# Optimization experiments

Measured on AMD Instinct MI355X. Metric: run time of the kernel, lower is better.

## Reference

```python
import jax, jax.numpy as jnp
import numpy as np

G, M_PER_GROUP, K, N = 8, 2048, 4096, 4096  # experts, tokens/expert, d_model, expert out dim


def setup_inputs() -> dict:
    key = jax.random.key(0)
    k1, k2, k3, k4 = jax.random.split(key, 4)
    T = G * M_PER_GROUP
    # int8 quantized activations [total_tokens, K] and per-expert weights [G, N, K] ('NT' layout)
    i8_left_tensor = jax.random.randint(k1, (T, K), -127, 128, dtype=jnp.int32).astype(jnp.int8)
    i8_right_tensors = jax.random.randint(k2, (G, N, K), -127, 128, dtype=jnp.int32).astype(jnp.int8)
    # per-token and per-(group, out-channel) dequant scales
    left_scales = jax.random.uniform(k3, (T,), jnp.float32, 0.001, 0.02)
    right_scales = jax.random.uniform(k4, (G, N), jnp.float32, 0.001, 0.02)
    tokens_per_group = jnp.full((G,), M_PER_GROUP, dtype=jnp.int32)
    return {
        "i8_left_tensor": i8_left_tensor,
        "i8_right_tensors": i8_right_tensors,
        "left_scales": left_scales,
        "right_scales": right_scales,
        "tokens_per_group": tokens_per_group,
    }


def reference(i8_left_tensor, i8_right_tensors, left_scales, right_scales, tokens_per_group):
    # moe_w8a8_group_gemm, 'NT': per group g, out_g = (A_g @ B_g^T) * ls_g[:, None] * rs_g[None, :] -> fp16
    g, n, k = i8_right_tensors.shape
    t = i8_left_tensor.shape[0]
    m = t // g  # equal-sized groups (tokens_per_group is constant M_PER_GROUP)
    a = i8_left_tensor.reshape(g, m, k).astype(jnp.float32)   # [G, M, K]
    b = i8_right_tensors.astype(jnp.float32)                  # [G, N, K]
    acc = jnp.einsum('gmk,gnk->gmn', a, b)                    # int8xint8 accum in f32
    ls = left_scales.reshape(g, m, 1)
    rs = right_scales[:, None, :]
    out = (acc * ls * rs).astype(jnp.float16)                 # fused dequant epilogue
    return out.reshape(t, n)
```

## Files before the change

### kernel.cpp

```cpp
#include <hip/hip_runtime.h>

#define GG 8
#define MPG 2048
#define KD 4096
#define ND 4096

using i32x4 = __attribute__((ext_vector_type(4))) int;

__device__ __forceinline__ int pack4(i32x4 v) {
  return (int)((unsigned)(v[0] & 0xff) | ((unsigned)(v[1] & 0xff) << 8) |
               ((unsigned)(v[2] & 0xff) << 16) | ((unsigned)(v[3] & 0xff) << 24));
}

__global__ void conv_kernel(const int* __restrict__ src, char* __restrict__ dst, long nelem) {
  long t = (long)blockIdx.x * blockDim.x + threadIdx.x;
  long stride = (long)gridDim.x * blockDim.x;
  for (long e = t * 16; e < nelem; e += stride * 16) {
    i32x4 x0 = *(const i32x4*)(src + e);
    i32x4 x1 = *(const i32x4*)(src + e + 4);
    i32x4 x2 = *(const i32x4*)(src + e + 8);
    i32x4 x3 = *(const i32x4*)(src + e + 12);
    i32x4 p;
    p[0] = pack4(x0); p[1] = pack4(x1); p[2] = pack4(x2); p[3] = pack4(x3);
    *(i32x4*)(dst + e) = p;
  }
}

__device__ __forceinline__ void gload_lds16(const void* g, void* l) {
  __builtin_amdgcn_global_load_lds(
      (const __attribute__((address_space(1))) unsigned int*)g,
      (__attribute__((address_space(3))) unsigned int*)l, 16, 0, 0);
}

#define CFENCE() asm volatile("" ::: "memory")

constexpr int NT = KD / 128;

__global__ __launch_bounds__(512, 2) void gemm256_i8(
    const char* __restrict__ Aall,
    const char* __restrict__ Ball,
    const float* __restrict__ ls,
    const float* __restrict__ rs,
    float* __restrict__ out,
    int g0, int nwg)
{
  extern __shared__ char lds[];

  const int tid  = threadIdx.x;
  const int lane = tid & 63;
  const int wave = tid >> 6;

  int bid = blockIdx.x;
  int wg  = (bid & 7) * (nwg >> 3) + (bid >> 3);
  const int gl = wg >> 7;
  const int rr_ = wg & 127;
  const int bm = (rr_ >> 4) * 256;
  const int bn = (rr_ & 15) * 256;
  const int g  = g0 + gl;

  const int srow = tid >> 3;
  const int scol = ((tid & 7) << 4) ^ ((srow & 7) << 4);
  const char* Ag = Aall + ((size_t)gl * MPG + bm) * KD;
  const char* Bg = Ball + ((size_t)gl * ND  + bn) * KD;
  const char* pa[4]; const char* pb[4];
#pragma unroll
  for (int i = 0; i < 4; ++i) {
    pa[i] = Ag + (size_t)(i * 64 + srow) * KD + scol;
    pb[i] = Bg + (size_t)(i * 64 + srow) * KD + scol;
  }
  char* wbase = lds + wave * 1024;

  auto stageA = [&](int buf, int kt) {
    const int ko = kt << 7;
    char* d = wbase + buf * 65536;
#pragma unroll
    for (int i = 0; i < 4; ++i) gload_lds16(pa[i] + ko, d + i * 8192);
  };
  auto stageB = [&](int buf, int kt) {
    const int ko = kt << 7;
    char* d = wbase + buf * 65536 + 32768;
#pragma unroll
    for (int i = 0; i < 4; ++i) gload_lds16(pb[i] + ko, d + i * 8192);
  };

  const int wm = wave >> 2;
  const int wn = wave & 3;
  const int r16 = lane & 15;
  const int klane = (lane >> 4) << 4;
  const int sx = (r16 & 7) << 4;
  const char* aBase0 = lds + (size_t)(wm * 128 + r16) * 128;
  const char* bBase0 = lds + 32768 + (size_t)(wn * 64 + r16) * 128;

  i32x4 acc[8][4] = {};

  stageA(0, 0); stageB(0, 0);
  asm volatile("s_waitcnt vmcnt(0)" ::: "memory");
  __builtin_amdgcn_s_barrier();
  CFENCE();

#pragma unroll 1
  for (int kt = 0; kt < NT; ++kt) {
    const int c = kt & 1;
    const char* pA = aBase0 + c * 65536;
    const char* pB = bBase0 + c * 65536;
    const int kx0 = klane ^ sx;
    const int kx1 = (64 + klane) ^ sx;
    const bool pre = (kt + 1 < NT);
    i32x4 af[4], bf[4];

#pragma unroll
    for (int n = 0; n < 4; ++n) bf[n] = *(const i32x4*)(pB + n * 2048 + kx0);
#pragma unroll
    for (int m = 0; m < 4; ++m) af[m] = *(const i32x4*)(pA + m * 2048 + kx0);
    if (pre) stageA(c ^ 1, kt + 1);
    CFENCE(); __builtin_amdgcn_s_barrier(); CFENCE();
    __builtin_amdgcn_s_setprio(1);
#pragma unroll
    for (int m = 0; m < 4; ++m)
#pragma unroll
      for (int n = 0; n < 4; ++n)
        acc[m][n] = __builtin_amdgcn_mfma_i32_16x16x64_i8(af[m], bf[n], acc[m][n], 0, 0, 0);
    __builtin_amdgcn_s_setprio(0);
    CFENCE(); __builtin_amdgcn_s_barrier(); CFENCE();

#pragma unroll
    for (int m = 0; m < 4; ++m) af[m] = *(const i32x4*)(pA + (4 + m) * 2048 + kx0);
    if (pre) stageB(c ^ 1, kt + 1);
    CFENCE(); __builtin_amdgcn_s_barrier(); CFENCE();
    __builtin_amdgcn_s_setprio(1);
#pragma unroll
    for (int m = 0; m < 4; ++m)
#pragma unroll
      for (int n = 0; n < 4; ++n)
        acc[4 + m][n] = __builtin_amdgcn_mfma_i32_16x16x64_i8(af[m], bf[n], acc[4 + m][n], 0, 0, 0);
    __builtin_amdgcn_s_setprio(0);
    CFENCE(); __builtin_amdgcn_s_barrier(); CFENCE();

#pragma unroll
    for (int n = 0; n < 4; ++n) bf[n] = *(const i32x4*)(pB + n * 2048 + kx1);
#pragma unroll
    for (int m = 0; m < 4; ++m) af[m] = *(const i32x4*)(pA + m * 2048 + kx1);
    CFENCE(); __builtin_amdgcn_s_barrier(); CFENCE();
    __builtin_amdgcn_s_setprio(1);
#pragma unroll
    for (int m = 0; m < 4; ++m)
#pragma unroll
      for (int n = 0; n < 4; ++n)
        acc[m][n] = __builtin_amdgcn_mfma_i32_16x16x64_i8(af[m], bf[n], acc[m][n], 0, 0, 0);
    __builtin_amdgcn_s_setprio(0);
    CFENCE(); __builtin_amdgcn_s_barrier(); CFENCE();

#pragma unroll
    for (int m = 0; m < 4; ++m) af[m] = *(const i32x4*)(pA + (4 + m) * 2048 + kx1);
    asm volatile("s_waitcnt vmcnt(0)" ::: "memory");
    CFENCE(); __builtin_amdgcn_s_barrier(); CFENCE();
    __builtin_amdgcn_s_setprio(1);
#pragma unroll
    for (int m = 0; m < 4; ++m)
#pragma unroll
      for (int n = 0; n < 4; ++n)
        acc[4 + m][n] = __builtin_amdgcn_mfma_i32_16x16x64_i8(af[m], bf[n], acc[4 + m][n], 0, 0, 0);
    __builtin_amdgcn_s_setprio(0);
    CFENCE(); __builtin_amdgcn_s_barrier(); CFENCE();
  }

  const size_t orow0 = (size_t)g * MPG + bm + wm * 128 + ((lane >> 4) << 2);
  const int col0 = bn + wn * 64 + r16;
  float rsv[4];
#pragma unroll
  for (int n = 0; n < 4; ++n) rsv[n] = rs[(size_t)g * ND + col0 + n * 16];
#pragma unroll
  for (int m = 0; m < 8; ++m) {
#pragma unroll
    for (int q = 0; q < 4; ++q) {
      size_t row = orow0 + m * 16 + q;
      float lsv = ls[row];
#pragma unroll
      for (int n = 0; n < 4; ++n)
        out[row * ND + col0 + n * 16] = (float)acc[m][n][q] * lsv * rsv[n];
    }
  }
}

constexpr int BM = 128, BN = 128, BK = 64;

template<bool DIRECT>
__global__ __launch_bounds__(256) void gemm_i8(
    const void* __restrict__ Aptr, const void* __restrict__ Bptr,
    const float* __restrict__ ls, const float* __restrict__ rs,
    float* __restrict__ out, int g0)
{
  __shared__ char lA[BM * BK];
  __shared__ char lB[BN * BK];

  const int gl = blockIdx.z;
  const int g = g0 + gl;
  const int bm = blockIdx.y * BM;
  const int bn = blockIdx.x * BN;
  const int tid = threadIdx.x;
  const int lane = tid & 63;
  const int wave = tid >> 6;
  const int wr = (wave >> 1) * 64;
  const int wc = (wave & 1) * 64;
  const int r16 = lane & 15;
  const int kb = (lane >> 4) * 16;

  i32x4 acc[4][4] = {};

  if constexpr (!DIRECT) {
    const char* Ag = (const char*)Aptr + ((size_t)gl * MPG + bm) * KD;
    const char* Bg = (const char*)Bptr + ((size_t)gl * ND + bn) * KD;
    const int srow = tid >> 2;
    const int skoff = (tid & 3) * 16;
    const char* pa0 = Ag + (size_t)srow * KD + skoff;
    const char* pa1 = Ag + (size_t)(srow + 64) * KD + skoff;
    const char* pb0 = Bg + (size_t)srow * KD + skoff;
    const char* pb1 = Bg + (size_t)(srow + 64) * KD + skoff;
    char* la0 = lA + wave * 1024;
    char* la1 = lA + 4096 + wave * 1024;
    char* lb0 = lB + wave * 1024;
    char* lb1 = lB + 4096 + wave * 1024;

    for (int k0 = 0; k0 < KD; k0 += BK) {
      gload_lds16(pa0 + k0, la0);
      gload_lds16(pa1 + k0, la1);
      gload_lds16(pb0 + k0, lb0);
      gload_lds16(pb1 + k0, lb1);
      __syncthreads();
      i32x4 af[4], bf[4];
#pragma unroll
      for (int m = 0; m < 4; ++m) af[m] = *(const i32x4*)(lA + (wr + m * 16 + r16) * BK + kb);
#pragma unroll
      for (int n = 0; n < 4; ++n) bf[n] = *(const i32x4*)(lB + (wc + n * 16 + r16) * BK + kb);
#pragma unroll
      for (int m = 0; m < 4; ++m)
#pragma unroll
        for (int n = 0; n < 4; ++n)
          acc[m][n] = __builtin_amdgcn_mfma_i32_16x16x64_i8(af[m], bf[n], acc[m][n], 0, 0, 0);
      __syncthreads();
    }
  } else {
    const int* Ag = (const int*)Aptr + ((size_t)gl * MPG + bm) * KD;
    const int* Bg = (const int*)Bptr + ((size_t)gl * ND + bn) * KD;
    const int drow = tid >> 1;
    const int dk = (tid & 1) * 32;

    for (int k0 = 0; k0 < KD; k0 += BK) {
      int pa[8], pb[8];
#pragma unroll
      for (int j = 0; j < 8; ++j) pa[j] = pack4(*(const i32x4*)(Ag + (size_t)drow * KD + k0 + dk + j * 4));
#pragma unroll
      for (int j = 0; j < 8; ++j) pb[j] = pack4(*(const i32x4*)(Bg + (size_t)drow * KD + k0 + dk + j * 4));
      __syncthreads();
      *(i32x4*)(lA + drow * 64 + dk)      = *(i32x4*)(pa);
      *(i32x4*)(lA + drow * 64 + dk + 16) = *(i32x4*)(pa + 4);
      *(i32x4*)(lB + drow * 64 + dk)      = *(i32x4*)(pb);
      *(i32x4*)(lB + drow * 64 + dk + 16) = *(i32x4*)(pb + 4);
      __syncthreads();
      i32x4 af[4], bf[4];
#pragma unroll
      for (int m = 0; m < 4; ++m) af[m] = *(const i32x4*)(lA + (wr + m * 16 + r16) * BK + kb);
#pragma unroll
      for (int n = 0; n < 4; ++n) bf[n] = *(const i32x4*)(lB + (wc + n * 16 + r16) * BK + kb);
#pragma unroll
      for (int m = 0; m < 4; ++m)
#pragma unroll
        for (int n = 0; n < 4; ++n)
          acc[m][n] = __builtin_amdgcn_mfma_i32_16x16x64_i8(af[m], bf[n], acc[m][n], 0, 0, 0);
    }
  }

  const size_t trow0 = (size_t)g * MPG + bm + wr + (lane >> 4) * 4;
  const int col0 = bn + wc + r16;
  float rsv[4];
#pragma unroll
  for (int n = 0; n < 4; ++n) rsv[n] = rs[(size_t)g * ND + col0 + n * 16];
#pragma unroll
  for (int m = 0; m < 4; ++m) {
#pragma unroll
    for (int q = 0; q < 4; ++q) {
      size_t row = trow0 + m * 16 + q;
      float lsv = ls[row];
#pragma unroll
      for (int n = 0; n < 4; ++n)
        out[row * ND + col0 + n * 16] = (float)acc[m][n][q] * lsv * rsv[n];
    }
  }
}

extern "C" void kernel_launch(void* const* d_in, const int* in_sizes, int n_in,
                              void* d_out, int out_size, void* d_ws, size_t ws_size,
                              hipStream_t stream) {
  const int* A32 = (const int*)d_in[0];
  const int* B32 = (const int*)d_in[1];
  const float* ls = (const float*)d_in[2];
  const float* rs = (const float*)d_in[3];
  float* out = (float*)d_out;

  const size_t aE = (size_t)GG * MPG * KD;
  const size_t bE = (size_t)GG * ND * KD;
  const size_t aSlab = (size_t)MPG * KD;
  const size_t bSlab = (size_t)ND * KD;

  const int smem = 131072;
  bool big_lds_ok =
      hipFuncSetAttribute((const void*)gemm256_i8,
                          hipFuncAttributeMaxDynamicSharedMemorySize, smem) == hipSuccess;

  if (d_ws && ws_size >= aE + bE) {
    char* wsA = (char*)d_ws;
    char* wsB = wsA + aE;
    conv_kernel<<<8192, 256, 0, stream>>>(A32, wsA, (long)aE);
    conv_kernel<<<16384, 256, 0, stream>>>(B32, wsB, (long)bE);
    if (big_lds_ok) {
      gemm256_i8<<<1024, 512, smem, stream>>>(wsA, wsB, ls, rs, out, 0, 1024);
    } else {
      dim3 grid(ND / BN, MPG / BM, GG);
      gemm_i8<false><<<grid, dim3(256), 0, stream>>>(wsA, wsB, ls, rs, out, 0);
    }
  } else if (d_ws && ws_size >= aSlab + bSlab) {
    char* wsA = (char*)d_ws;
    char* wsB = wsA + aSlab;
    for (int gidx = 0; gidx < GG; ++gidx) {
      conv_kernel<<<2048, 256, 0, stream>>>(A32 + (size_t)gidx * aSlab, wsA, (long)aSlab);
      conv_kernel<<<4096, 256, 0, stream>>>(B32 + (size_t)gidx * bSlab, wsB, (long)bSlab);
      if (big_lds_ok) {
        gemm256_i8<<<128, 512, smem, stream>>>(wsA, wsB, ls, rs, out, gidx, 128);
      } else {
        dim3 grid(ND / BN, MPG / BM, 1);
        gemm_i8<false><<<grid, dim3(256), 0, stream>>>(wsA, wsB, ls, rs, out, gidx);
      }
    }
  } else {
    dim3 grid(ND / BN, MPG / BM, GG);
    gemm_i8<true><<<grid, dim3(256), 0, stream>>>(A32, B32, ls, rs, out, 0);
  }
}
```

Measured before the change: 484.5 us.

## Deepen global-to-LDS prefetch to two tiles ahead and cut barriers per k-step

Restructures the main loop so global-to-LDS loads for tile kt+2 are issued at the end of iteration kt, instead of staging the next tile halfway through the current one. Each iteration now waits on vmcnt(8) and a single barrier up front, then runs all four MFMA sub-blocks with extra fragment registers (double A/B fragments) in place of eight interleaved barriers. The aim is to hide global latency better and remove barrier stalls, at the cost of more VGPRs. It relies on the vmcnt count matching exactly the number of outstanding loads for one tile, and on the buffer being reused only after every wave has finished reading it.

```diff
diff --git a/kernel.cpp b/kernel.cpp
--- a/kernel.cpp
+++ b/kernel.cpp
@@ -94,9 +94,7 @@
   i32x4 acc[8][4] = {};
 
   stageA(0, 0); stageB(0, 0);
-  asm volatile("s_waitcnt vmcnt(0)" ::: "memory");
-  __builtin_amdgcn_s_barrier();
-  CFENCE();
+  stageA(1, 1); stageB(1, 1);
 
 #pragma unroll 1
   for (int kt = 0; kt < NT; ++kt) {
@@ -105,63 +103,57 @@
     const char* pB = bBase0 + c * 65536;
     const int kx0 = klane ^ sx;
     const int kx1 = (64 + klane) ^ sx;
-    const bool pre = (kt + 1 < NT);
-    i32x4 af[4], bf[4];
-
-#pragma unroll
-    for (int n = 0; n < 4; ++n) bf[n] = *(const i32x4*)(pB + n * 2048 + kx0);
-#pragma unroll
-    for (int m = 0; m < 4; ++m) af[m] = *(const i32x4*)(pA + m * 2048 + kx0);
-    if (pre) stageA(c ^ 1, kt + 1);
-    CFENCE(); __builtin_amdgcn_s_barrier(); CFENCE();
+
+    if (kt + 1 < NT) { asm volatile("s_waitcnt vmcnt(8)" ::: "memory"); }
+    else             { asm volatile("s_waitcnt vmcnt(0)" ::: "memory"); }
+    __builtin_amdgcn_s_barrier();
+    CFENCE();
+
+    i32x4 bf0[4], bf1[4], af0[4], af1[4];
+#pragma unroll
+    for (int n = 0; n < 4; ++n) bf0[n] = *(const i32x4*)(pB + n * 2048 + kx0);
+#pragma unroll
+    for (int m = 0; m < 4; ++m) af0[m] = *(const i32x4*)(pA + m * 2048 + kx0);
+#pragma unroll
+    for (int m = 0; m < 4; ++m) af1[m] = *(const i32x4*)(pA + (4 + m) * 2048 + kx0);
     __builtin_amdgcn_s_setprio(1);
 #pragma unroll
     for (int m = 0; m < 4; ++m)
 #pragma unroll
       for (int n = 0; n < 4; ++n)
-        acc[m][n] = __builtin_amdgcn_mfma_i32_16x16x64_i8(af[m], bf[n], acc[m][n], 0, 0, 0);
+        acc[m][n] = __builtin_amdgcn_mfma_i32_16x16x64_i8(af0[m], bf0[n], acc[m][n], 0, 0, 0);
     __builtin_amdgcn_s_setprio(0);
-    CFENCE(); __builtin_amdgcn_s_barrier(); CFENCE();
-
-#pragma unroll
-    for (int m = 0; m < 4; ++m) af[m] = *(const i32x4*)(pA + (4 + m) * 2048 + kx0);
-    if (pre) stageB(c ^ 1, kt + 1);
-    CFENCE(); __builtin_amdgcn_s_barrier(); CFENCE();
+#pragma unroll
+    for (int n = 0; n < 4; ++n) bf1[n] = *(const i32x4*)(pB + n * 2048 + kx1);
+#pragma unroll
+    for (int m = 0; m < 4; ++m) af0[m] = *(const i32x4*)(pA + m * 2048 + kx1);
     __builtin_amdgcn_s_setprio(1);
 #pragma unroll
     for (int m = 0; m < 4; ++m)
 #pragma unroll
       for (int n = 0; n < 4; ++n)
-        acc[4 + m][n] = __builtin_amdgcn_mfma_i32_16x16x64_i8(af[m], bf[n], acc[4 + m][n], 0, 0, 0);
+        acc[4 + m][n] = __builtin_amdgcn_mfma_i32_16x16x64_i8(af1[m], bf0[n], acc[4 + m][n], 0, 0, 0);
     __builtin_amdgcn_s_setprio(0);
-    CFENCE(); __builtin_amdgcn_s_barrier(); CFENCE();
-
-#pragma unroll
-    for (int n = 0; n < 4; ++n) bf[n] = *(const i32x4*)(pB + n * 2048 + kx1);
-#pragma unroll
-    for (int m = 0; m < 4; ++m) af[m] = *(const i32x4*)(pA + m * 2048 + kx1);
-    CFENCE(); __builtin_amdgcn_s_barrier(); CFENCE();
+#pragma unroll
+    for (int m = 0; m < 4; ++m) af1[m] = *(const i32x4*)(pA + (4 + m) * 2048 + kx1);
     __builtin_amdgcn_s_setprio(1);
 #pragma unroll
     for (int m = 0; m < 4; ++m)
 #pragma unroll
       for (int n = 0; n < 4; ++n)
-        acc[m][n] = __builtin_amdgcn_mfma_i32_16x16x64_i8(af[m], bf[n], acc[m][n], 0, 0, 0);
+        acc[m][n] = __builtin_amdgcn_mfma_i32_16x16x64_i8(af0[m], bf1[n], acc[m][n], 0, 0, 0);
+#pragma unroll
+    for (int m = 0; m < 4; ++m)
+#pragma unroll
+      for (int n = 0; n < 4; ++n)
+        acc[4 + m][n] = __builtin_amdgcn_mfma_i32_16x16x64_i8(af1[m], bf1[n], acc[4 + m][n], 0, 0, 0);
     __builtin_amdgcn_s_setprio(0);
-    CFENCE(); __builtin_amdgcn_s_barrier(); CFENCE();
-
-#pragma unroll
-    for (int m = 0; m < 4; ++m) af[m] = *(const i32x4*)(pA + (4 + m) * 2048 + kx1);
-    asm volatile("s_waitcnt vmcnt(0)" ::: "memory");
-    CFENCE(); __builtin_amdgcn_s_barrier(); CFENCE();
-    __builtin_amdgcn_s_setprio(1);
-#pragma unroll
-    for (int m = 0; m < 4; ++m)
-#pragma unroll
-      for (int n = 0; n < 4; ++n)
-        acc[4 + m][n] = __builtin_amdgcn_mfma_i32_16x16x64_i8(af[m], bf[n], acc[4 + m][n], 0, 0, 0);
-    __builtin_amdgcn_s_setprio(0);
-    CFENCE(); __builtin_amdgcn_s_barrier(); CFENCE();
+
+    asm volatile("s_waitcnt lgkmcnt(0)" ::: "memory");
+    __builtin_amdgcn_sched_barrier(0);
+    __builtin_amdgcn_s_barrier();
+    CFENCE();
+    if (kt + 2 < NT) { stageA(c, kt + 2); stageB(c, kt + 2); }
   }
 
   const size_t orow0 = (size_t)g * MPG + bm + wm * 128 + ((lane >> 4) << 2);
```

New measurement: 496.6 us. 2.5% more time.

## Fuse int8 conversion and grouped GEMM into one cooperative persistent kernel

Applied to the files above, without the earlier changes.

Replaces the separate conversion and GEMM launches with a single cooperative kernel. 128 blocks pack the int32 inputs to int8 group by group and publish per-group completion flags, while 384 persistent blocks run 256x128 tiles and spin-wait on those flags, so conversion of later groups overlaps GEMM on earlier ones. The new tile uses a single LDS buffer with 256 threads (48KB LDS), making stage loads synchronous with compute, and relies on atomic flag polling with a bounded spin. Fewer GEMM blocks and no double buffering could reduce GEMM throughput compared with the previous 512-thread double-buffered kernel.

```diff
diff --git a/kernel.cpp b/kernel.cpp
--- a/kernel.cpp
+++ b/kernel.cpp
@@ -12,18 +12,20 @@
                ((unsigned)(v[2] & 0xff) << 16) | ((unsigned)(v[3] & 0xff) << 24));
 }
 
+__device__ __forceinline__ void pack16(const int* __restrict__ src, char* __restrict__ dst, long e) {
+  i32x4 x0 = *(const i32x4*)(src + e);
+  i32x4 x1 = *(const i32x4*)(src + e + 4);
+  i32x4 x2 = *(const i32x4*)(src + e + 8);
+  i32x4 x3 = *(const i32x4*)(src + e + 12);
+  i32x4 p;
+  p[0] = pack4(x0); p[1] = pack4(x1); p[2] = pack4(x2); p[3] = pack4(x3);
+  *(i32x4*)(dst + e) = p;
+}
+
 __global__ void conv_kernel(const int* __restrict__ src, char* __restrict__ dst, long nelem) {
   long t = (long)blockIdx.x * blockDim.x + threadIdx.x;
-  long stride = (long)gridDim.x * blockDim.x;
-  for (long e = t * 16; e < nelem; e += stride * 16) {
-    i32x4 x0 = *(const i32x4*)(src + e);
-    i32x4 x1 = *(const i32x4*)(src + e + 4);
-    i32x4 x2 = *(const i32x4*)(src + e + 8);
-    i32x4 x3 = *(const i32x4*)(src + e + 12);
-    i32x4 p;
-    p[0] = pack4(x0); p[1] = pack4(x1); p[2] = pack4(x2); p[3] = pack4(x3);
-    *(i32x4*)(dst + e) = p;
-  }
+  long stride = (long)gridDim.x * blockDim.x * 16;
+  for (long e = t * 16; e < nelem; e += stride) pack16(src, dst, e);
 }
 
 __device__ __forceinline__ void gload_lds16(const void* g, void* l) {
@@ -34,34 +36,210 @@
 
 #define CFENCE() asm volatile("" ::: "memory")
 
-constexpr int NT = KD / 128;
-
-__global__ __launch_bounds__(512, 2) void gemm256_i8(
-    const char* __restrict__ Aall,
-    const char* __restrict__ Ball,
-    const float* __restrict__ ls,
-    const float* __restrict__ rs,
-    float* __restrict__ out,
-    int g0, int nwg)
+constexpr long A_EL = (long)MPG * KD;
+constexpr long B_EL = (long)ND * KD;
+constexpr int NTK = KD / 128;
+constexpr int NGEMM_B = 384;
+constexpr int NCONV_B = 128;
+constexpr int NTILES = GG * 256;
+
+__device__ __forceinline__ void gemm_tile(
+    char* lds, const char* __restrict__ Ag8, const char* __restrict__ Bg8,
+    const float* __restrict__ ls, const float* __restrict__ rs,
+    float* __restrict__ out, int g, int bm, int bn)
+{
+  const int tid = threadIdx.x;
+  const int lane = tid & 63;
+  const int wave = tid >> 6;
+
+  const int srow = tid >> 3;
+  const int scol = ((tid & 7) << 4) ^ ((srow & 7) << 4);
+  const char* Ag = Ag8 + (size_t)bm * KD;
+  const char* Bg = Bg8 + (size_t)bn * KD;
+  const int voff = srow * KD + scol;
+  char* wbase = lds + wave * 1024;
+
+  auto stage = [&](int kt) {
+    const int ko = kt << 7;
+#pragma unroll
+    for (int i = 0; i < 8; ++i)
+      gload_lds16(Ag + (size_t)(ko + voff) + (size_t)i * (32 * KD), wbase + i * 4096);
+#pragma unroll
+    for (int i = 0; i < 4; ++i)
+      gload_lds16(Bg + (size_t)(ko + voff) + (size_t)i * (32 * KD), wbase + 32768 + i * 4096);
+  };
+
+  const int wm = wave >> 1;
+  const int wn = wave & 1;
+  const int r16 = lane & 15;
+  const int klane = (lane >> 4) << 4;
+  const int sx = (r16 & 7) << 4;
+  const char* pA = lds + (size_t)(wm * 128 + r16) * 128;
+  const char* pB = lds + 32768 + (size_t)(wn * 64 + r16) * 128;
+  const int kx0 = klane ^ sx;
+  const int kx1 = (64 + klane) ^ sx;
+
+  i32x4 acc[8][4] = {};
+
+  stage(0);
+  asm volatile("s_waitcnt vmcnt(0)" ::: "memory");
+  __builtin_amdgcn_s_barrier();
+  CFENCE();
+
+#pragma unroll 1
+  for (int kt = 0; kt < NTK; ++kt) {
+    i32x4 bf0[4], bf1[4], af0[4], af1[4];
+#pragma unroll
+    for (int n = 0; n < 4; ++n) bf0[n] = *(const i32x4*)(pB + n * 2048 + kx0);
+#pragma unroll
+    for (int m = 0; m < 4; ++m) af0[m] = *(const i32x4*)(pA + m * 2048 + kx0);
+#pragma unroll
+    for (int m = 0; m < 4; ++m) af1[m] = *(const i32x4*)(pA + (4 + m) * 2048 + kx0);
+    __builtin_amdgcn_s_setprio(1);
+#pragma unroll
+    for (int m = 0; m < 4; ++m)
+#pragma unroll
+      for (int n = 0; n < 4; ++n)
+        acc[m][n] = __builtin_amdgcn_mfma_i32_16x16x64_i8(af0[m], bf0[n], acc[m][n], 0, 0, 0);
+    __builtin_amdgcn_s_setprio(0);
+#pragma unroll
+    for (int n = 0; n < 4; ++n) bf1[n] = *(const i32x4*)(pB + n * 2048 + kx1);
+#pragma unroll
+    for (int m = 0; m < 4; ++m) af0[m] = *(const i32x4*)(pA + m * 2048 + kx1);
+    __builtin_amdgcn_s_setprio(1);
+#pragma unroll
+    for (int m = 0; m < 4; ++m)
+#pragma unroll
+      for (int n = 0; n < 4; ++n)
+        acc[4 + m][n] = __builtin_amdgcn_mfma_i32_16x16x64_i8(af1[m], bf0[n], acc[4 + m][n], 0, 0, 0);
+    __builtin_amdgcn_s_setprio(0);
+#pragma unroll
+    for (int m = 0; m < 4; ++m) af1[m] = *(const i32x4*)(pA + (4 + m) * 2048 + kx1);
+    __builtin_amdgcn_s_setprio(1);
+#pragma unroll
+    for (int m = 0; m < 4; ++m)
+#pragma unroll
+      for (int n = 0; n < 4; ++n)
+        acc[m][n] = __builtin_amdgcn_mfma_i32_16x16x64_i8(af0[m], bf1[n], acc[m][n], 0, 0, 0);
+#pragma unroll
+    for (int m = 0; m < 4; ++m)
+#pragma unroll
+      for (int n = 0; n < 4; ++n)
+        acc[4 + m][n] = __builtin_amdgcn_mfma_i32_16x16x64_i8(af1[m], bf1[n], acc[4 + m][n], 0, 0, 0);
+    __builtin_amdgcn_s_setprio(0);
+
+    asm volatile("s_waitcnt lgkmcnt(0)" ::: "memory");
+    __builtin_amdgcn_sched_barrier(0);
+    __builtin_amdgcn_s_barrier();
+    CFENCE();
+    if (kt + 1 < NTK) stage(kt + 1);
+    asm volatile("s_waitcnt vmcnt(0)" ::: "memory");
+    __builtin_amdgcn_s_barrier();
+    CFENCE();
+  }
+
+  const size_t orow0 = (size_t)g * MPG + bm + wm * 128 + ((lane >> 4) << 2);
+  const int col0 = bn + wn * 64 + r16;
+  float rsv[4];
+#pragma unroll
+  for (int n = 0; n < 4; ++n) rsv[n] = rs[(size_t)g * ND + col0 + n * 16];
+#pragma unroll
+  for (int m = 0; m < 8; ++m) {
+#pragma unroll
+    for (int q = 0; q < 4; ++q) {
+      size_t row = orow0 + m * 16 + q;
+      float lsv = ls[row];
+#pragma unroll
+      for (int n = 0; n < 4; ++n)
+        out[row * ND + col0 + n * 16] = (float)acc[m][n][q] * lsv * rsv[n];
+    }
+  }
+}
+
+__global__ __launch_bounds__(256, 2) void mega_i8(
+    const int* __restrict__ A32, const int* __restrict__ B32,
+    char* __restrict__ wsA, char* __restrict__ wsB,
+    const float* __restrict__ ls, const float* __restrict__ rs,
+    float* __restrict__ out, int* __restrict__ flags)
 {
   extern __shared__ char lds[];
-
-  const int tid  = threadIdx.x;
+  const int tid = threadIdx.x;
+
+  if (blockIdx.x >= NGEMM_B) {
+    const int cb = blockIdx.x - NGEMM_B;
+    const long nthr = (long)NCONV_B * 256;
+    const long t0 = (long)cb * 256 + tid;
+    for (int g = 0; g < GG; ++g) {
+      {
+        const int* src = A32 + (size_t)g * A_EL;
+        char* dst = wsA + (size_t)g * A_EL;
+        for (long e = t0 * 64; e < A_EL; e += nthr * 64) {
+          pack16(src, dst, e);      pack16(src, dst, e + 16);
+          pack16(src, dst, e + 32); pack16(src, dst, e + 48);
+        }
+      }
+      {
+        const int* src = B32 + (size_t)g * B_EL;
+        char* dst = wsB + (size_t)g * B_EL;
+        for (long e = t0 * 64; e < B_EL; e += nthr * 64) {
+          pack16(src, dst, e);      pack16(src, dst, e + 16);
+          pack16(src, dst, e + 32); pack16(src, dst, e + 48);
+        }
+      }
+      __threadfence();
+      __syncthreads();
+      if (tid == 0) {
+        if (atomicAdd(&flags[1 + g], 1) == NCONV_B - 1)
+          atomicAdd(&flags[0], 1);
+      }
+    }
+    return;
+  }
+
+  const int b = blockIdx.x;
+  const int bs = (b & 7) * (NGEMM_B / 8) + (b >> 3);
+#pragma unroll 1
+  for (int t = bs; t < NTILES; t += NGEMM_B) {
+    const int grp = t >> 8;
+    const int idx = t & 255;
+    const int bm = (idx >> 5) * 256;
+    const int bn = (idx & 31) * 128;
+    if (tid == 0) {
+      int cap = 0;
+      while (atomicAdd(&flags[0], 0) < grp + 1) {
+        __builtin_amdgcn_s_sleep(2);
+        if (++cap > 5000000) break;
+      }
+    }
+    __syncthreads();
+    __threadfence();
+    gemm_tile(lds, wsA + (size_t)grp * A_EL, wsB + (size_t)grp * B_EL,
+              ls, rs, out, grp, bm, bn);
+  }
+}
+
+__global__ __launch_bounds__(512, 2) void gemm256sq_i8(
+    const char* __restrict__ Aall, const char* __restrict__ Ball,
+    const float* __restrict__ ls, const float* __restrict__ rs,
+    float* __restrict__ out, int g0, int nwg)
+{
+  extern __shared__ char lds[];
+  const int tid = threadIdx.x;
   const int lane = tid & 63;
   const int wave = tid >> 6;
 
   int bid = blockIdx.x;
-  int wg  = (bid & 7) * (nwg >> 3) + (bid >> 3);
+  int wg = (bid & 7) * (nwg >> 3) + (bid >> 3);
   const int gl = wg >> 7;
   const int rr_ = wg & 127;
   const int bm = (rr_ >> 4) * 256;
   const int bn = (rr_ & 15) * 256;
-  const int g  = g0 + gl;
+  const int g = g0 + gl;
 
   const int srow = tid >> 3;
   const int scol = ((tid & 7) << 4) ^ ((srow & 7) << 4);
   const char* Ag = Aall + ((size_t)gl * MPG + bm) * KD;
-  const char* Bg = Ball + ((size_t)gl * ND  + bn) * KD;
+  const char* Bg = Ball + ((size_t)gl * ND + bn) * KD;
   const char* pa[4]; const char* pb[4];
 #pragma unroll
   for (int i = 0; i < 4; ++i) {
@@ -99,13 +277,13 @@
   CFENCE();
 
 #pragma unroll 1
-  for (int kt = 0; kt < NT; ++kt) {
+  for (int kt = 0; kt < NTK; ++kt) {
     const int c = kt & 1;
     const char* pA = aBase0 + c * 65536;
     const char* pB = bBase0 + c * 65536;
     const int kx0 = klane ^ sx;
     const int kx1 = (64 + klane) ^ sx;
-    const bool pre = (kt + 1 < NT);
+    const bool pre = (kt + 1 < NTK);
     i32x4 af[4], bf[4];
 
 #pragma unroll
@@ -174,112 +352,6 @@
 #pragma unroll
     for (int q = 0; q < 4; ++q) {
       size_t row = orow0 + m * 16 + q;
-      float lsv = ls[row];
-#pragma unroll
-      for (int n = 0; n < 4; ++n)
-        out[row * ND + col0 + n * 16] = (float)acc[m][n][q] * lsv * rsv[n];
-    }
-  }
-}
-
-constexpr int BM = 128, BN = 128, BK = 64;
-
-template<bool DIRECT>
-__global__ __launch_bounds__(256) void gemm_i8(
-    const void* __restrict__ Aptr, const void* __restrict__ Bptr,
-    const float* __restrict__ ls, const float* __restrict__ rs,
-    float* __restrict__ out, int g0)
-{
-  __shared__ char lA[BM * BK];
-  __shared__ char lB[BN * BK];
-
-  const int gl = blockIdx.z;
-  const int g = g0 + gl;
-  const int bm = blockIdx.y * BM;
-  const int bn = blockIdx.x * BN;
-  const int tid = threadIdx.x;
-  const int lane = tid & 63;
-  const int wave = tid >> 6;
-  const int wr = (wave >> 1) * 64;
-  const int wc = (wave & 1) * 64;
-  const int r16 = lane & 15;
-  const int kb = (lane >> 4) * 16;
-
-  i32x4 acc[4][4] = {};
-
-  if constexpr (!DIRECT) {
-    const char* Ag = (const char*)Aptr + ((size_t)gl * MPG + bm) * KD;
-    const char* Bg = (const char*)Bptr + ((size_t)gl * ND + bn) * KD;
-    const int srow = tid >> 2;
-    const int skoff = (tid & 3) * 16;
-    const char* pa0 = Ag + (size_t)srow * KD + skoff;
-    const char* pa1 = Ag + (size_t)(srow + 64) * KD + skoff;
-    const char* pb0 = Bg + (size_t)srow * KD + skoff;
-    const char* pb1 = Bg + (size_t)(srow + 64) * KD + skoff;
-    char* la0 = lA + wave * 1024;
-    char* la1 = lA + 4096 + wave * 1024;
-    char* lb0 = lB + wave * 1024;
-    char* lb1 = lB + 4096 + wave * 1024;
-
-    for (int k0 = 0; k0 < KD; k0 += BK) {
-      gload_lds16(pa0 + k0, la0);
-      gload_lds16(pa1 + k0, la1);
-      gload_lds16(pb0 + k0, lb0);
-      gload_lds16(pb1 + k0, lb1);
-      __syncthreads();
-      i32x4 af[4], bf[4];
-#pragma unroll
-      for (int m = 0; m < 4; ++m) af[m] = *(const i32x4*)(lA + (wr + m * 16 + r16) * BK + kb);
-#pragma unroll
-      for (int n = 0; n < 4; ++n) bf[n] = *(const i32x4*)(lB + (wc + n * 16 + r16) * BK + kb);
-#pragma unroll
-      for (int m = 0; m < 4; ++m)
-#pragma unroll
-        for (int n = 0; n < 4; ++n)
-          acc[m][n] = __builtin_amdgcn_mfma_i32_16x16x64_i8(af[m], bf[n], acc[m][n], 0, 0, 0);
-      __syncthreads();
-    }
-  } else {
-    const int* Ag = (const int*)Aptr + ((size_t)gl * MPG + bm) * KD;
-    const int* Bg = (const int*)Bptr + ((size_t)gl * ND + bn) * KD;
-    const int drow = tid >> 1;
-    const int dk = (tid & 1) * 32;
-
-    for (int k0 = 0; k0 < KD; k0 += BK) {
-      int pa[8], pb[8];
-#pragma unroll
-      for (int j = 0; j < 8; ++j) pa[j] = pack4(*(const i32x4*)(Ag + (size_t)drow * KD + k0 + dk + j * 4));
-#pragma unroll
-      for (int j = 0; j < 8; ++j) pb[j] = pack4(*(const i32x4*)(Bg + (size_t)drow * KD + k0 + dk + j * 4));
-      __syncthreads();
-      *(i32x4*)(lA + drow * 64 + dk)      = *(i32x4*)(pa);
-      *(i32x4*)(lA + drow * 64 + dk + 16) = *(i32x4*)(pa + 4);
-      *(i32x4*)(lB + drow * 64 + dk)      = *(i32x4*)(pb);
-      *(i32x4*)(lB + drow * 64 + dk + 16) = *(i32x4*)(pb + 4);
-      __syncthreads();
-      i32x4 af[4], bf[4];
-#pragma unroll
-      for (int m = 0; m < 4; ++m) af[m] = *(const i32x4*)(lA + (wr + m * 16 + r16) * BK + kb);
-#pragma unroll
-      for (int n = 0; n < 4; ++n) bf[n] = *(const i32x4*)(lB + (wc + n * 16 + r16) * BK + kb);
-#pragma unroll
-      for (int m = 0; m < 4; ++m)
-#pragma unroll
-        for (int n = 0; n < 4; ++n)
-          acc[m][n] = __builtin_amdgcn_mfma_i32_16x16x64_i8(af[m], bf[n], acc[m][n], 0, 0, 0);
-    }
-  }
-
-  const size_t trow0 = (size_t)g * MPG + bm + wr + (lane >> 4) * 4;
-  const int col0 = bn + wc + r16;
-  float rsv[4];
-#pragma unroll
-  for (int n = 0; n < 4; ++n) rsv[n] = rs[(size_t)g * ND + col0 + n * 16];
-#pragma unroll
-  for (int m = 0; m < 4; ++m) {
-#pragma unroll
-    for (int q = 0; q < 4; ++q) {
-      size_t row = trow0 + m * 16 + q;
       float lsv = ls[row];
 #pragma unroll
       for (int n = 0; n < 4; ++n)
@@ -297,42 +369,63 @@
   const float* rs = (const float*)d_in[3];
   float* out = (float*)d_out;
 
-  const size_t aE = (size_t)GG * MPG * KD;
-  const size_t bE = (size_t)GG * ND * KD;
-  const size_t aSlab = (size_t)MPG * KD;
-  const size_t bSlab = (size_t)ND * KD;
-
-  const int smem = 131072;
-  bool big_lds_ok =
-      hipFuncSetAttribute((const void*)gemm256_i8,
-                          hipFuncAttributeMaxDynamicSharedMemorySize, smem) == hipSuccess;
+  const size_t aE = (size_t)GG * A_EL;
+  const size_t bE = (size_t)GG * B_EL;
+
+  if (d_ws && ws_size >= aE + bE + 64) {
+    int dev = 0;
+    hipGetDevice(&dev);
+    int coop = 0;
+    hipDeviceGetAttribute(&coop, hipDeviceAttributeCooperativeLaunch, dev);
+    if (coop) {
+      if (hipFuncSetAttribute((const void*)mega_i8,
+                              hipFuncAttributeMaxDynamicSharedMemorySize,
+                              49152) == hipSuccess) {
+        int nb = 0;
+        hipOccupancyMaxActiveBlocksPerMultiprocessor(&nb, (const void*)mega_i8, 256, 49152);
+        hipDeviceProp_t prop;
+        hipGetDeviceProperties(&prop, dev);
+        if ((long)nb * prop.multiProcessorCount >= NGEMM_B + NCONV_B) {
+          char* wsA = (char*)d_ws;
+          char* wsB = wsA + aE;
+          int* flags = (int*)(wsA + aE + bE);
+          hipMemsetAsync(flags, 0, 64, stream);
+          const int* a32 = A32; const int* b32 = B32;
+          const float* lsp = ls; const float* rsp = rs;
+          float* outp = out;
+          void* args[] = {(void*)&a32, (void*)&b32, (void*)&wsA, (void*)&wsB,
+                          (void*)&lsp, (void*)&rsp, (void*)&outp, (void*)&flags};
+          hipError_t e = hipLaunchCooperativeKernel(
+              (const void*)mega_i8, dim3(NGEMM_B + NCONV_B), dim3(256),
+              args, 49152, stream);
+          if (e == hipSuccess) return;
+        }
+      }
+    }
+  }
 
   if (d_ws && ws_size >= aE + bE) {
     char* wsA = (char*)d_ws;
     char* wsB = wsA + aE;
     conv_kernel<<<8192, 256, 0, stream>>>(A32, wsA, (long)aE);
     conv_kernel<<<16384, 256, 0, stream>>>(B32, wsB, (long)bE);
-    if (big_lds_ok) {
-      gemm256_i8<<<1024, 512, smem, stream>>>(wsA, wsB, ls, rs, out, 0, 1024);
-    } else {
-      dim3 grid(ND / BN, MPG / BM, GG);
-      gemm_i8<false><<<grid, dim3(256), 0, stream>>>(wsA, wsB, ls, rs, out, 0);
-    }
-  } else if (d_ws && ws_size >= aSlab + bSlab) {
+    if (hipFuncSetAttribute((const void*)gemm256sq_i8,
+                            hipFuncAttributeMaxDynamicSharedMemorySize,
+                            131072) == hipSuccess) {
+      gemm256sq_i8<<<1024, 512, 131072, stream>>>(wsA, wsB, ls, rs, out, 0, 1024);
+      return;
+    }
+  }
+
+  if (d_ws && ws_size >= (size_t)(A_EL + B_EL)) {
     char* wsA = (char*)d_ws;
-    char* wsB = wsA + aSlab;
-    for (int gidx = 0; gidx < GG; ++gidx) {
-      conv_kernel<<<2048, 256, 0, stream>>>(A32 + (size_t)gidx * aSlab, wsA, (long)aSlab);
-      conv_kernel<<<4096, 256, 0, stream>>>(B32 + (size_t)gidx * bSlab, wsB, (long)bSlab);
-      if (big_lds_ok) {
-        gemm256_i8<<<128, 512, smem, stream>>>(wsA, wsB, ls, rs, out, gidx, 128);
-      } else {
-        dim3 grid(ND / BN, MPG / BM, 1);
-        gemm_i8<false><<<grid, dim3(256), 0, stream>>>(wsA, wsB, ls, rs, out, gidx);
-      }
-    }
-  } else {
-    dim3 grid(ND / BN, MPG / BM, GG);
-    gemm_i8<true><<<grid, dim3(256), 0, stream>>>(A32, B32, ls, rs, out, 0);
-  }
-}
+    char* wsB = wsA + A_EL;
+    hipFuncSetAttribute((const void*)gemm256sq_i8,
+                        hipFuncAttributeMaxDynamicSharedMemorySize, 131072);
+    for (int g = 0; g < GG; ++g) {
+      conv_kernel<<<2048, 256, 0, stream>>>(A32 + (size_t)g * A_EL, wsA, (long)A_EL);
+      conv_kernel<<<4096, 256, 0, stream>>>(B32 + (size_t)g * B_EL, wsB, (long)B_EL);
+      gemm256sq_i8<<<128, 512, 131072, stream>>>(wsA, wsB, ls, rs, out, g, 128);
+    }
+  }
+}
```

After: 487.6 us. No clear change (+0.7%).

## Fuse int32-to-int8 packing into the GEMM load path and drop conversion kernels

Applied to the files above, without the earlier changes.

The GEMM kernel now reads the int32-stored operands directly from global memory into registers, packs them to int8 in-kernel, and writes them to swizzled LDS, replacing the async global_load_lds path that read pre-converted int8 buffers. The two separate conversion kernels and their workspace round-trip are skipped whenever large LDS is available. Loads for the next k-tile are issued in quarters between MFMA phases to overlap. In exchange, each GEMM tile now reads 4x the bytes from global memory and uses extra VGPRs for staging, which may cut occupancy or expose memory latency.

```diff
diff --git a/kernel.cpp b/kernel.cpp
--- a/kernel.cpp
+++ b/kernel.cpp
@@ -14,8 +14,8 @@
 
 __global__ void conv_kernel(const int* __restrict__ src, char* __restrict__ dst, long nelem) {
   long t = (long)blockIdx.x * blockDim.x + threadIdx.x;
-  long stride = (long)gridDim.x * blockDim.x;
-  for (long e = t * 16; e < nelem; e += stride * 16) {
+  long stride = (long)gridDim.x * blockDim.x * 16;
+  for (long e = t * 16; e < nelem; e += stride) {
     i32x4 x0 = *(const i32x4*)(src + e);
     i32x4 x1 = *(const i32x4*)(src + e + 4);
     i32x4 x2 = *(const i32x4*)(src + e + 8);
@@ -36,13 +36,13 @@
 
 constexpr int NT = KD / 128;
 
-__global__ __launch_bounds__(512, 2) void gemm256_i8(
-    const char* __restrict__ Aall,
-    const char* __restrict__ Ball,
+__global__ __launch_bounds__(512, 2) void gemmf_i8(
+    const int* __restrict__ A32,
+    const int* __restrict__ B32,
     const float* __restrict__ ls,
     const float* __restrict__ rs,
     float* __restrict__ out,
-    int g0, int nwg)
+    int nwg)
 {
   extern __shared__ char lds[];
 
@@ -56,31 +56,34 @@
   const int rr_ = wg & 127;
   const int bm = (rr_ >> 4) * 256;
   const int bn = (rr_ & 15) * 256;
-  const int g  = g0 + gl;
 
   const int srow = tid >> 3;
-  const int scol = ((tid & 7) << 4) ^ ((srow & 7) << 4);
-  const char* Ag = Aall + ((size_t)gl * MPG + bm) * KD;
-  const char* Bg = Ball + ((size_t)gl * ND  + bn) * KD;
-  const char* pa[4]; const char* pb[4];
-#pragma unroll
-  for (int i = 0; i < 4; ++i) {
-    pa[i] = Ag + (size_t)(i * 64 + srow) * KD + scol;
-    pb[i] = Bg + (size_t)(i * 64 + srow) * KD + scol;
-  }
-  char* wbase = lds + wave * 1024;
-
-  auto stageA = [&](int buf, int kt) {
+  const int lincol = (tid & 7) * 16;
+  const int sxw = (srow & 7) << 4;
+  const int* a32 = A32 + ((size_t)gl * MPG + bm) * KD;
+  const int* b32 = B32 + ((size_t)gl * ND + bn) * KD;
+
+  i32x4 sreg[8];
+
+  auto issue_half = [&](int kt, int mat, int h) {
     const int ko = kt << 7;
-    char* d = wbase + buf * 65536;
-#pragma unroll
-    for (int i = 0; i < 4; ++i) gload_lds16(pa[i] + ko, d + i * 8192);
+    const int* src = mat ? b32 : a32;
+#pragma unroll
+    for (int ii = 0; ii < 2; ++ii)
+#pragma unroll
+      for (int j = 0; j < 4; ++j)
+        sreg[ii * 4 + j] = *(const i32x4*)(src + (size_t)((h * 2 + ii) * 64 + srow) * KD
+                                               + ko + lincol + j * 4);
   };
-  auto stageB = [&](int buf, int kt) {
-    const int ko = kt << 7;
-    char* d = wbase + buf * 65536 + 32768;
-#pragma unroll
-    for (int i = 0; i < 4; ++i) gload_lds16(pb[i] + ko, d + i * 8192);
+  auto write_half = [&](int buf, int mat, int h) {
+    char* dstb = lds + buf * 65536 + mat * 32768;
+#pragma unroll
+    for (int ii = 0; ii < 2; ++ii) {
+      i32x4 p;
+      p[0] = pack4(sreg[ii * 4 + 0]); p[1] = pack4(sreg[ii * 4 + 1]);
+      p[2] = pack4(sreg[ii * 4 + 2]); p[3] = pack4(sreg[ii * 4 + 3]);
+      *(i32x4*)(dstb + (size_t)((h * 2 + ii) * 64 + srow) * 128 + (lincol ^ sxw)) = p;
+    }
   };
 
   const int wm = wave >> 2;
@@ -88,23 +91,26 @@
   const int r16 = lane & 15;
   const int klane = (lane >> 4) << 4;
   const int sx = (r16 & 7) << 4;
-  const char* aBase0 = lds + (size_t)(wm * 128 + r16) * 128;
-  const char* bBase0 = lds + 32768 + (size_t)(wn * 64 + r16) * 128;
+  const int aoff = (wm * 128 + r16) * 128;
+  const int boff = 32768 + (wn * 64 + r16) * 128;
+  const int kx0 = klane ^ sx;
+  const int kx1 = (64 + klane) ^ sx;
 
   i32x4 acc[8][4] = {};
 
-  stageA(0, 0); stageB(0, 0);
-  asm volatile("s_waitcnt vmcnt(0)" ::: "memory");
+  issue_half(0, 0, 0); write_half(0, 0, 0);
+  issue_half(0, 0, 1); write_half(0, 0, 1);
+  issue_half(0, 1, 0); write_half(0, 1, 0);
+  issue_half(0, 1, 1); write_half(0, 1, 1);
+  asm volatile("s_waitcnt lgkmcnt(0)" ::: "memory");
   __builtin_amdgcn_s_barrier();
   CFENCE();
 
 #pragma unroll 1
   for (int kt = 0; kt < NT; ++kt) {
     const int c = kt & 1;
-    const char* pA = aBase0 + c * 65536;
-    const char* pB = bBase0 + c * 65536;
-    const int kx0 = klane ^ sx;
-    const int kx1 = (64 + klane) ^ sx;
+    const char* pA = lds + c * 65536 + aoff;
+    const char* pB = lds + c * 65536 + boff;
     const bool pre = (kt + 1 < NT);
     i32x4 af[4], bf[4];
 
@@ -112,7 +118,7 @@
     for (int n = 0; n < 4; ++n) bf[n] = *(const i32x4*)(pB + n * 2048 + kx0);
 #pragma unroll
     for (int m = 0; m < 4; ++m) af[m] = *(const i32x4*)(pA + m * 2048 + kx0);
-    if (pre) stageA(c ^ 1, kt + 1);
+    if (pre) issue_half(kt + 1, 0, 0);
     CFENCE(); __builtin_amdgcn_s_barrier(); CFENCE();
     __builtin_amdgcn_s_setprio(1);
 #pragma unroll
@@ -121,11 +127,12 @@
       for (int n = 0; n < 4; ++n)
         acc[m][n] = __builtin_amdgcn_mfma_i32_16x16x64_i8(af[m], bf[n], acc[m][n], 0, 0, 0);
     __builtin_amdgcn_s_setprio(0);
+    if (pre) write_half(c ^ 1, 0, 0);
     CFENCE(); __builtin_amdgcn_s_barrier(); CFENCE();
 
 #pragma unroll
     for (int m = 0; m < 4; ++m) af[m] = *(const i32x4*)(pA + (4 + m) * 2048 + kx0);
-    if (pre) stageB(c ^ 1, kt + 1);
+    if (pre) issue_half(kt + 1, 0, 1);
     CFENCE(); __builtin_amdgcn_s_barrier(); CFENCE();
     __builtin_amdgcn_s_setprio(1);
 #pragma unroll
@@ -134,12 +141,14 @@
       for (int n = 0; n < 4; ++n)
         acc[4 + m][n] = __builtin_amdgcn_mfma_i32_16x16x64_i8(af[m], bf[n], acc[4 + m][n], 0, 0, 0);
     __builtin_amdgcn_s_setprio(0);
+    if (pre) write_half(c ^ 1, 0, 1);
     CFENCE(); __builtin_amdgcn_s_barrier(); CFENCE();
 
 #pragma unroll
     for (int n = 0; n < 4; ++n) bf[n] = *(const i32x4*)(pB + n * 2048 + kx1);
 #pragma unroll
     for (int m = 0; m < 4; ++m) af[m] = *(const i32x4*)(pA + m * 2048 + kx1);
+    if (pre) issue_half(kt + 1, 1, 0);
     CFENCE(); __builtin_amdgcn_s_barrier(); CFENCE();
     __builtin_amdgcn_s_setprio(1);
 #pragma unroll
@@ -148,11 +157,12 @@
       for (int n = 0; n < 4; ++n)
         acc[m][n] = __builtin_amdgcn_mfma_i32_16x16x64_i8(af[m], bf[n], acc[m][n], 0, 0, 0);
     __builtin_amdgcn_s_setprio(0);
+    if (pre) write_half(c ^ 1, 1, 0);
     CFENCE(); __builtin_amdgcn_s_barrier(); CFENCE();
 
 #pragma unroll
     for (int m = 0; m < 4; ++m) af[m] = *(const i32x4*)(pA + (4 + m) * 2048 + kx1);
-    asm volatile("s_waitcnt vmcnt(0)" ::: "memory");
+    if (pre) issue_half(kt + 1, 1, 1);
     CFENCE(); __builtin_amdgcn_s_barrier(); CFENCE();
     __builtin_amdgcn_s_setprio(1);
 #pragma unroll
@@ -161,14 +171,18 @@
       for (int n = 0; n < 4; ++n)
         acc[4 + m][n] = __builtin_amdgcn_mfma_i32_16x16x64_i8(af[m], bf[n], acc[4 + m][n], 0, 0, 0);
     __builtin_amdgcn_s_setprio(0);
-    CFENCE(); __builtin_amdgcn_s_barrier(); CFENCE();
-  }
-
-  const size_t orow0 = (size_t)g * MPG + bm + wm * 128 + ((lane >> 4) << 2);
+    if (pre) write_half(c ^ 1, 1, 1);
+    asm volatile("s_waitcnt lgkmcnt(0)" ::: "memory");
+    __builtin_amdgcn_sched_barrier(0);
+    __builtin_amdgcn_s_barrier();
+    CFENCE();
+  }
+
+  const size_t orow0 = (size_t)gl * MPG + bm + wm * 128 + ((lane >> 4) << 2);
   const int col0 = bn + wn * 64 + r16;
   float rsv[4];
 #pragma unroll
-  for (int n = 0; n < 4; ++n) rsv[n] = rs[(size_t)g * ND + col0 + n * 16];
+  for (int n = 0; n < 4; ++n) rsv[n] = rs[(size_t)gl * ND + col0 + n * 16];
 #pragma unroll
   for (int m = 0; m < 8; ++m) {
 #pragma unroll
@@ -302,34 +316,28 @@
   const size_t aSlab = (size_t)MPG * KD;
   const size_t bSlab = (size_t)ND * KD;
 
-  const int smem = 131072;
-  bool big_lds_ok =
-      hipFuncSetAttribute((const void*)gemm256_i8,
-                          hipFuncAttributeMaxDynamicSharedMemorySize, smem) == hipSuccess;
+  if (hipFuncSetAttribute((const void*)gemmf_i8,
+                          hipFuncAttributeMaxDynamicSharedMemorySize,
+                          131072) == hipSuccess) {
+    gemmf_i8<<<1024, 512, 131072, stream>>>(A32, B32, ls, rs, out, 1024);
+    return;
+  }
 
   if (d_ws && ws_size >= aE + bE) {
     char* wsA = (char*)d_ws;
     char* wsB = wsA + aE;
     conv_kernel<<<8192, 256, 0, stream>>>(A32, wsA, (long)aE);
     conv_kernel<<<16384, 256, 0, stream>>>(B32, wsB, (long)bE);
-    if (big_lds_ok) {
-      gemm256_i8<<<1024, 512, smem, stream>>>(wsA, wsB, ls, rs, out, 0, 1024);
-    } else {
-      dim3 grid(ND / BN, MPG / BM, GG);
-      gemm_i8<false><<<grid, dim3(256), 0, stream>>>(wsA, wsB, ls, rs, out, 0);
-    }
+    dim3 grid(ND / BN, MPG / BM, GG);
+    gemm_i8<false><<<grid, dim3(256), 0, stream>>>(wsA, wsB, ls, rs, out, 0);
   } else if (d_ws && ws_size >= aSlab + bSlab) {
     char* wsA = (char*)d_ws;
     char* wsB = wsA + aSlab;
     for (int gidx = 0; gidx < GG; ++gidx) {
       conv_kernel<<<2048, 256, 0, stream>>>(A32 + (size_t)gidx * aSlab, wsA, (long)aSlab);
       conv_kernel<<<4096, 256, 0, stream>>>(B32 + (size_t)gidx * bSlab, wsB, (long)bSlab);
-      if (big_lds_ok) {
-        gemm256_i8<<<128, 512, smem, stream>>>(wsA, wsB, ls, rs, out, gidx, 128);
-      } else {
-        dim3 grid(ND / BN, MPG / BM, 1);
-        gemm_i8<false><<<grid, dim3(256), 0, stream>>>(wsA, wsB, ls, rs, out, gidx);
-      }
+      dim3 grid(ND / BN, MPG / BM, 1);
+      gemm_i8<false><<<grid, dim3(256), 0, stream>>>(wsA, wsB, ls, rs, out, gidx);
     }
   } else {
     dim3 grid(ND / BN, MPG / BM, GG);
```

New measurement: 973.4 us. 101% more time.
